# Kernel tuning notes

Hardware: AMD Instinct MI355X
Metric: run time of the kernel (lower is better)

## Reference

```python
import jax, jax.numpy as jnp
import numpy as np

# config (matches SS2Dv2 defaults: d_model=96, d_state=16, ssm_ratio=2.0, dt_rank=auto=6, k_group=4)
DM, DI, N, K, R = 96, 192, 16, 4, 6
BSZ, H_, W_ = 1, 56, 56


def setup_inputs() -> dict:
    key = jax.random.key(0)
    ks = jax.random.split(key, 8)
    return {
        "x": jax.random.normal(ks[0], (BSZ, H_, W_, DM), jnp.float32),
        "in_proj_w": jax.random.normal(ks[1], (2 * DI, DM), jnp.float32) / np.sqrt(DM).astype(np.float32),
        "conv_w": jax.random.normal(ks[2], (DI, 1, 3, 3), jnp.float32) * 0.1,
        "conv_b": jnp.zeros((DI,), jnp.float32),
        "x_proj_w": jax.random.normal(ks[3], (K, R + 2 * N, DI), jnp.float32) / np.sqrt(DI).astype(np.float32),
        "dt_projs_w": 0.1 * jax.random.uniform(ks[4], (K, DI, R), jnp.float32),
        "dt_projs_bias": 0.1 * jax.random.uniform(ks[5], (K, DI), jnp.float32),
        "A_logs": jnp.zeros((K * DI, N), jnp.float32),
        "Ds": jnp.ones((K * DI,), jnp.float32),
        "ln_w": jnp.ones((DI,), jnp.float32),
        "ln_b": jnp.zeros((DI,), jnp.float32),
        "out_proj_w": jax.random.normal(ks[6], (DM, DI), jnp.float32) / np.sqrt(DI).astype(np.float32),
    }


def _cross_scan(x):
    # x: (B, D, H, W) -> (B, 4, D, L); dirs: row-major, col-major, and their flips
    B, D, H, W = x.shape
    L = H * W
    x0 = x.reshape(B, D, L)
    x1 = jnp.swapaxes(x, 2, 3).reshape(B, D, L)
    return jnp.stack([x0, x1, x0[..., ::-1], x1[..., ::-1]], axis=1)


def _cross_merge(ys, H, W):
    # ys: (B, K, D, L) -> (B, D, L); invert each scan direction and sum
    B, Kk, D, L = ys.shape
    y0 = ys[:, 0]
    y2 = ys[:, 2][..., ::-1]
    y1 = jnp.swapaxes(ys[:, 1].reshape(B, D, W, H), 2, 3).reshape(B, D, L)
    y3 = jnp.swapaxes(ys[:, 3][..., ::-1].reshape(B, D, W, H), 2, 3).reshape(B, D, L)
    return y0 + y1 + y2 + y3


def _forward(x, in_proj_w, conv_w, conv_b, x_proj_w, dt_projs_w, dt_projs_bias,
             A_logs, Ds, ln_w, ln_b, out_proj_w):
    B, H, W, _ = x.shape
    L = H * W
    # in_proj + gate split (channel_first=False -> last dim)
    xz = jnp.einsum('bhwc,oc->bhwo', x, in_proj_w)
    xc, z = jnp.split(xz, 2, axis=-1)
    z = jax.nn.silu(z)
    # depthwise conv (NCHW)
    xc = jnp.transpose(xc, (0, 3, 1, 2))
    xc = jax.lax.conv_general_dilated(
        xc, conv_w, (1, 1), 'SAME', feature_group_count=DI,
        dimension_numbers=('NCHW', 'OIHW', 'NCHW')) + conv_b[None, :, None, None]
    xc = jax.nn.silu(xc)
    # 4-directional cross scan
    xs = _cross_scan(xc)  # (B,K,D,L)
    # grouped x_proj: per direction D -> R+2N
    x_dbl = jnp.einsum('bkdl,krd->bkrl', xs, x_proj_w)
    dts, Bs, Cs = jnp.split(x_dbl, [R, R + N], axis=2)  # (B,K,R,L),(B,K,N,L),(B,K,N,L)
    # grouped dt proj: per direction R -> D
    dts = jnp.einsum('bkrl,kdr->bkdl', dts, dt_projs_w)
    A = -jnp.exp(A_logs.astype(jnp.float32)).reshape(K, DI, N)
    delta = jax.nn.softplus(dts + dt_projs_bias[None, :, :, None])  # (B,K,D,L)
    # S6 selective scan: h_t = exp(delta*A)*h_{t-1} + delta*B*u, y_t = C.h_t + D*u
    dA = jnp.exp(jnp.einsum('bkdl,kdn->bkdln', delta, A))
    dBu = jnp.einsum('bkdl,bknl,bkdl->bkdln', delta, Bs, xs)

    def comb(e1, e2):
        a1, b1 = e1
        a2, b2 = e2
        return a2 * a1, a2 * b1 + b2

    _, h = jax.lax.associative_scan(comb, (dA, dBu), axis=3)  # (B,K,D,L,N)
    y = jnp.einsum('bkdln,bknl->bkdl', h, Cs) + Ds.reshape(K, DI)[None, :, :, None] * xs
    y = _cross_merge(y, H, W).reshape(B, DI, H, W)
    # out_norm: LayerNorm over channels (channel_first=False path)
    y = jnp.transpose(y, (0, 2, 3, 1))  # (B,H,W,D)
    mu = y.mean(-1, keepdims=True)
    var = ((y - mu) ** 2).mean(-1, keepdims=True)
    y = (y - mu) / jnp.sqrt(var + 1e-5) * ln_w + ln_b
    y = y * z
    return jnp.einsum('bhwd,od->bhwo', y, out_proj_w)


def reference(x, in_proj_w, conv_w, conv_b, x_proj_w, dt_projs_w, dt_projs_bias,
              A_logs, Ds, ln_w, ln_b, out_proj_w):
    return _forward(x, in_proj_w, conv_w, conv_b, x_proj_w, dt_projs_w, dt_projs_bias,
                    A_logs, Ds, ln_w, ln_b, out_proj_w)
```

## Files before the change

### kernel.cpp

```cpp
#include <hip/hip_runtime.h>
#include <hip/hip_bf16.h>
#include <math.h>

#define DM 96
#define DI 192
#define NS 16
#define KK 4
#define RR 6
#define HH 56
#define WW 56
#define LL (HH*WW)
#define RN (RR + 2*NS)
#define NCH 64
#define CLL (LL/NCH)

__device__ __forceinline__ float silu_f(float x) { return x / (1.f + __expf(-x)); }
__device__ __forceinline__ float softplus_f(float x) {
    return (x > 20.f) ? x : log1pf(__expf(x));
}

__global__ __launch_bounds__(256) void k_inproj(
        const float* __restrict__ x, const float* __restrict__ w,
        float* __restrict__ xc_t, float* __restrict__ z_nat) {
    __shared__ float xt[32 * 100];
    __shared__ float wt[32 * 100];
    const int l0 = blockIdx.x * 32;
    const int o0 = blockIdx.y * 32;
    const int tid = threadIdx.x;
    for (int i = tid; i < 32 * 24; i += 256) {
        int r = i / 24, q = i % 24;
        *(float4*)&xt[r * 100 + 4 * q] = *(const float4*)&x[(size_t)(l0 + r) * DM + 4 * q];
        *(float4*)&wt[r * 100 + 4 * q] = *(const float4*)&w[(size_t)(o0 + r) * DM + 4 * q];
    }
    __syncthreads();
    const int tx = tid & 15, ty = tid >> 4;
    float acc[2][2] = {};
    for (int c = 0; c < 96; c += 4) {
        float4 av[2], bv[2];
#pragma unroll
        for (int i = 0; i < 2; ++i) av[i] = *(const float4*)&xt[(ty + 16 * i) * 100 + c];
#pragma unroll
        for (int j = 0; j < 2; ++j) bv[j] = *(const float4*)&wt[(tx + 16 * j) * 100 + c];
#pragma unroll
        for (int i = 0; i < 2; ++i)
#pragma unroll
            for (int j = 0; j < 2; ++j) {
                acc[i][j] = fmaf(av[i].x, bv[j].x, acc[i][j]);
                acc[i][j] = fmaf(av[i].y, bv[j].y, acc[i][j]);
                acc[i][j] = fmaf(av[i].z, bv[j].z, acc[i][j]);
                acc[i][j] = fmaf(av[i].w, bv[j].w, acc[i][j]);
            }
    }
    __syncthreads();
    float* ot = xt;
#pragma unroll
    for (int j = 0; j < 2; ++j)
#pragma unroll
        for (int i = 0; i < 2; ++i)
            ot[(tx + 16 * j) * 65 + (ty + 16 * i)] = acc[i][j];
    __syncthreads();
    if (o0 < DI) {
        for (int i = tid; i < 32 * 32; i += 256) {
            int ol = i >> 5, ll = i & 31;
            xc_t[(size_t)(o0 + ol) * LL + l0 + ll] = ot[ol * 65 + ll];
        }
    } else {
        for (int i = tid; i < 32 * 32; i += 256) {
            int ll = i >> 5, ol = i & 31;
            z_nat[(size_t)(l0 + ll) * DI + (o0 - DI) + ol] = silu_f(ot[ol * 65 + ll]);
        }
    }
}

__global__ __launch_bounds__(256) void k_convT(
        const float* __restrict__ xc_t, const float* __restrict__ cw,
        const float* __restrict__ cb, float* __restrict__ xconv, float* __restrict__ xs1) {
    __shared__ float in_s[16 * 56];
    __shared__ float out_s[14 * 57];
    const int d = blockIdx.x;
    const int h0 = blockIdx.y * 14;
    const int tid = threadIdx.x;
    const float* in = xc_t + (size_t)d * LL;
    for (int i = tid; i < 16 * 14; i += 256) {
        int row = i / 14, q = i % 14;
        int r = row - 1 + h0;
        float4 v = make_float4(0.f, 0.f, 0.f, 0.f);
        if (r >= 0 && r < HH) v = *(const float4*)&in[r * WW + 4 * q];
        *(float4*)&in_s[row * 56 + 4 * q] = v;
    }
    __syncthreads();
    const float b0 = cb[d];
    float w9[9];
#pragma unroll
    for (int i = 0; i < 9; ++i) w9[i] = cw[d * 9 + i];
    for (int i = tid; i < 14 * 56; i += 256) {
        int hh = i / 56, w = i % 56;
        float acc = b0;
#pragma unroll
        for (int di = 0; di < 3; ++di)
#pragma unroll
            for (int dj = 0; dj < 3; ++dj) {
                int w2 = w + dj - 1;
                if (w2 < 0 || w2 >= WW) continue;
                acc = fmaf(in_s[(hh + di) * 56 + w2], w9[di * 3 + dj], acc);
            }
        acc = silu_f(acc);
        xconv[(size_t)d * LL + (h0 + hh) * WW + w] = acc;
        out_s[hh * 57 + w] = acc;
    }
    __syncthreads();
    for (int i = tid; i < 14 * 56; i += 256) {
        int w = i / 14, hh = i % 14;
        xs1[(size_t)d * LL + w * HH + h0 + hh] = out_s[hh * 57 + w];
    }
}

__global__ __launch_bounds__(256) void k_xdblD(
        const float* __restrict__ xconv, const float* __restrict__ xs1,
        const float* __restrict__ pw, const float* __restrict__ dtw,
        const float* __restrict__ dtb,
        float* __restrict__ Bn, float* __restrict__ Cn, float* __restrict__ delta) {
    __shared__ float xt[DI * 16];
    __shared__ float wk_s[32 * DI];
    __shared__ float dtS[RR * 17];
    const int k = blockIdx.y;
    const int l0 = blockIdx.x * 16;
    const int tid = threadIdx.x;
    const float* in = (k & 1) ? xs1 : xconv;
    const float* wk = pw + (size_t)k * RN * DI;
    for (int i = tid; i < DI * 4; i += 256) {
        int d = i >> 2, q = i & 3;
        *(float4*)&xt[(d << 4) + 4 * q] = *(const float4*)&in[(size_t)d * LL + l0 + 4 * q];
    }
    {
        const float4* src = (const float4*)(wk + RR * DI);
        float4* dst = (float4*)wk_s;
        for (int i = tid; i < (32 * DI) / 4; i += 256) dst[i] = src[i];
    }
    __syncthreads();
    if (tid < RR * 16) {
        int r = tid >> 4, lx = tid & 15;
        const float* wr = wk + r * DI;
        float acc = 0.f;
#pragma unroll 8
        for (int d = 0; d < DI; ++d) acc = fmaf(xt[(d << 4) + lx], wr[d], acc);
        dtS[r * 17 + lx] = acc;
    }
    {
        const int sx = tid & 15, cg = tid >> 4;
        float acc2[2] = {};
        for (int d = 0; d < DI; d += 4) {
            float x0 = xt[(d + 0) * 16 + sx];
            float x1 = xt[(d + 1) * 16 + sx];
            float x2 = xt[(d + 2) * 16 + sx];
            float x3 = xt[(d + 3) * 16 + sx];
#pragma unroll
            for (int j = 0; j < 2; ++j) {
                float4 wv = *(const float4*)&wk_s[(cg + 16 * j) * DI + d];
                acc2[j] = fmaf(x0, wv.x, acc2[j]);
                acc2[j] = fmaf(x1, wv.y, acc2[j]);
                acc2[j] = fmaf(x2, wv.z, acc2[j]);
                acc2[j] = fmaf(x3, wv.w, acc2[j]);
            }
        }
        int s = l0 + sx;
        int ss = (k < 2) ? s : (LL - 1 - s);
        int cch = ss / CLL, ttl = ss - cch * CLL;
        size_t idx = ((size_t)k * LL + (size_t)ttl * NCH + cch) * NS + cg;
        Bn[idx] = acc2[0];
        Cn[idx] = acc2[1];
    }
    __syncthreads();
    for (int oi = tid; oi < DI * 16; oi += 256) {
        int d = oi >> 4, sl = oi & 15;
        int kd = k * DI + d;
        const float* wr = dtw + (size_t)kd * RR;
        float acc = dtb[kd];
#pragma unroll
        for (int r = 0; r < RR; ++r) acc = fmaf(dtS[r * 17 + sl], wr[r], acc);
        delta[(size_t)kd * LL + l0 + sl] = softplus_f(acc);
    }
}

template<int STP, bool TRANS>
__device__ __forceinline__ void scan_dir(
        const float* sDel, const float* sU,
        const float* __restrict__ pB, const float* __restrict__ pC,
        float4 An, float Dv, int c, int n,
        float* __restrict__ sP, float* __restrict__ sH,
        float* __restrict__ yo0,
        float* ysm,
        int im0) {
    float sd = 0.f;
    float4 h = make_float4(0.f, 0.f, 0.f, 0.f);
#pragma unroll 7
    for (int tl = 0; tl < CLL; ++tl) {
        float dl = sDel[STP * tl];
        float u  = sU[STP * tl];
        float4 Bv = *(const float4*)&pB[(size_t)tl * (NCH * NS)];
        float du = dl * u;
        h.x = fmaf(__builtin_amdgcn_exp2f(dl * An.x), h.x, du * Bv.x);
        h.y = fmaf(__builtin_amdgcn_exp2f(dl * An.y), h.y, du * Bv.y);
        h.z = fmaf(__builtin_amdgcn_exp2f(dl * An.z), h.z, du * Bv.z);
        h.w = fmaf(__builtin_amdgcn_exp2f(dl * An.w), h.w, du * Bv.w);
        sd += dl;
    }
    *(float4*)&sP[c * NS + 4 * n] = make_float4(
        __builtin_amdgcn_exp2f(sd * An.x), __builtin_amdgcn_exp2f(sd * An.y),
        __builtin_amdgcn_exp2f(sd * An.z), __builtin_amdgcn_exp2f(sd * An.w));
    *(float4*)&sH[c * NS + 4 * n] = h;
    __syncthreads();
    float4 hin = make_float4(0.f, 0.f, 0.f, 0.f);
    for (int cc = 0; cc < c; ++cc) {
        float4 P  = *(const float4*)&sP[cc * NS + 4 * n];
        float4 Hh = *(const float4*)&sH[cc * NS + 4 * n];
        hin.x = fmaf(P.x, hin.x, Hh.x);
        hin.y = fmaf(P.y, hin.y, Hh.y);
        hin.z = fmaf(P.z, hin.z, Hh.z);
        hin.w = fmaf(P.w, hin.w, Hh.w);
    }

    float4 h2 = hin;
    float yreg[13];
#pragma unroll 7
    for (int tl = 0; tl < CLL; ++tl) {
        float dl = sDel[STP * tl];
        float u  = sU[STP * tl];
        float4 Bv = *(const float4*)&pB[(size_t)tl * (NCH * NS)];
        float4 Cv = *(const float4*)&pC[(size_t)tl * (NCH * NS)];
        float du = dl * u;
        h2.x = fmaf(__builtin_amdgcn_exp2f(dl * An.x), h2.x, du * Bv.x);
        h2.y = fmaf(__builtin_amdgcn_exp2f(dl * An.y), h2.y, du * Bv.y);
        h2.z = fmaf(__builtin_amdgcn_exp2f(dl * An.z), h2.z, du * Bv.z);
        h2.w = fmaf(__builtin_amdgcn_exp2f(dl * An.w), h2.w, du * Bv.w);
        float acc = h2.x * Cv.x;
        acc = fmaf(h2.y, Cv.y, acc);
        acc = fmaf(h2.z, Cv.z, acc);
        acc = fmaf(h2.w, Cv.w, acc);
        acc += __shfl_xor(acc, 2, 64);
        acc += __shfl_xor(acc, 1, 64);
        acc = fmaf(Dv, u, acc);
        if ((tl & 3) == n) yreg[tl >> 2] = acc;
    }
    if (!TRANS) {
#pragma unroll
        for (int j = 0; j < 12; ++j)
            yo0[STP * (j * 4 + n)] = yreg[j];
        if (n == 0)
            yo0[STP * 48] = yreg[12];
    } else {
        __syncthreads();
#pragma unroll
        for (int j = 0; j < 12; ++j) {
            int im = im0 + STP * (j * 4 + n);
            int w = im / HH, hh = im - w * HH;
            ysm[hh * 57 + w] = yreg[j];
        }
        if (n == 0) {
            int im = im0 + STP * 48;
            int w = im / HH, hh = im - w * HH;
            ysm[hh * 57 + w] = yreg[12];
        }
    }
}

__global__ __launch_bounds__(256) void k_scan(
        const float* __restrict__ delta, const float* __restrict__ Bn,
        const float* __restrict__ Cn,
        const float* __restrict__ xconv, const float* __restrict__ xs1,
        const float* __restrict__ A_logs, const float* __restrict__ Ds,
        float* __restrict__ y4) {
    __shared__ float sbuf[2 * LL];
    __shared__ float sP[NCH * NS];
    __shared__ float sH[NCH * NS];
    int b = blockIdx.x;
    int k = b / DI, d = b % DI;
    int tid = threadIdx.x;
    int c = tid >> 2, n = tid & 3;
    int kd = k * DI + d;
    const float LOG2E = 1.4426950408889634f;
    float4 Alg = *(const float4*)&A_logs[kd * NS + 4 * n];
    float4 An = make_float4(-__expf(Alg.x) * LOG2E, -__expf(Alg.y) * LOG2E,
                            -__expf(Alg.z) * LOG2E, -__expf(Alg.w) * LOG2E);
    float Dv = Ds[kd];
    const float* del = delta + (size_t)kd * LL;
    const float* uP  = ((k & 1) ? xs1 : xconv) + (size_t)d * LL;
    {
        const float4* s1 = (const float4*)del;
        const float4* s2 = (const float4*)uP;
        float4* d1 = (float4*)sbuf;
        float4* d2 = (float4*)(sbuf + LL);
        for (int i = tid; i < LL / 4; i += 256) {
            d1[i] = s1[i];
            d2[i] = s2[i];
        }
    }
    __syncthreads();
    const float* Bb = Bn + (size_t)k * LL * NS + c * NS + 4 * n;
    const float* Cb = Cn + (size_t)k * LL * NS + c * NS + 4 * n;
    float* yo = y4 + (size_t)kd * LL;
    const int t0 = c * CLL;
    const int imF = t0;
    const int imR = LL - 1 - t0;
    if (k == 0) {
        scan_dir<1, false>(sbuf + imF, sbuf + LL + imF, Bb, Cb,
                           An, Dv, c, n, sP, sH, yo + imF, nullptr, 0);
    } else if (k == 1) {
        scan_dir<1, true>(sbuf + imF, sbuf + LL + imF, Bb, Cb,
                          An, Dv, c, n, sP, sH, nullptr, sbuf, imF);
    } else if (k == 2) {
        scan_dir<-1, false>(sbuf + imR, sbuf + LL + imR, Bb, Cb,
                            An, Dv, c, n, sP, sH, yo + imR, nullptr, 0);
    } else {
        scan_dir<-1, true>(sbuf + imR, sbuf + LL + imR, Bb, Cb,
                           An, Dv, c, n, sP, sH, nullptr, sbuf, imR);
    }
    if (k & 1) {
        __syncthreads();
        for (int p = tid; p < LL; p += 256)
            yo[p] = sbuf[p + p / WW];
    }
}

__global__ __launch_bounds__(256) void k_lnout(
        const float* __restrict__ y4, const float* __restrict__ z_nat,
        const float* __restrict__ lnw, const float* __restrict__ lnb,
        const float* __restrict__ ow, float* __restrict__ out) {
    __shared__ float yv[16 * 196];
    __shared__ float ow_s[48 * 196];
    __shared__ float mean_s[16], inv_s[16];
    const int l0 = blockIdx.x * 16;
    const int tid = threadIdx.x;
    for (int i = tid; i < DI * 4; i += 256) {
        int d = i >> 2, q = i & 3;
        size_t off = (size_t)d * LL + l0 + 4 * q;
        float4 a = *(const float4*)&y4[off];
        float4 b = *(const float4*)&y4[(size_t)DI * LL + off];
        float4 c2 = *(const float4*)&y4[(size_t)(2 * DI) * LL + off];
        float4 e = *(const float4*)&y4[(size_t)(3 * DI) * LL + off];
        int p = 4 * q;
        yv[(p + 0) * 196 + d] = a.x + b.x + c2.x + e.x;
        yv[(p + 1) * 196 + d] = a.y + b.y + c2.y + e.y;
        yv[(p + 2) * 196 + d] = a.z + b.z + c2.z + e.z;
        yv[(p + 3) * 196 + d] = a.w + b.w + c2.w + e.w;
    }
    __syncthreads();
    {
        int p = tid >> 4, e = tid & 15;
        float s1 = 0.f;
#pragma unroll
        for (int m = 0; m < 12; ++m) s1 += yv[p * 196 + e + 16 * m];
        s1 += __shfl_xor(s1, 8, 64);
        s1 += __shfl_xor(s1, 4, 64);
        s1 += __shfl_xor(s1, 2, 64);
        s1 += __shfl_xor(s1, 1, 64);
        float mean = s1 * (1.f / DI);
        float s2 = 0.f;
#pragma unroll
        for (int m = 0; m < 12; ++m) {
            float dv = yv[p * 196 + e + 16 * m] - mean;
            s2 = fmaf(dv, dv, s2);
        }
        s2 += __shfl_xor(s2, 8, 64);
        s2 += __shfl_xor(s2, 4, 64);
        s2 += __shfl_xor(s2, 2, 64);
        s2 += __shfl_xor(s2, 1, 64);
        if (e == 0) {
            mean_s[p] = mean;
            inv_s[p] = rsqrtf(s2 * (1.f / DI) + 1e-5f);
        }
    }
    __syncthreads();
    for (int i = tid; i < 16 * 48; i += 256) {
        int p = i / 48, q = i % 48;
        float4 z4 = *(const float4*)&z_nat[(size_t)(l0 + p) * DI + 4 * q];
        float4 w4 = *(const float4*)&lnw[4 * q];
        float4 b4 = *(const float4*)&lnb[4 * q];
        float4 yy = *(const float4*)&yv[p * 196 + 4 * q];
        float m = mean_s[p], iv = inv_s[p];
        yy.x = ((yy.x - m) * iv * w4.x + b4.x) * z4.x;
        yy.y = ((yy.y - m) * iv * w4.y + b4.y) * z4.y;
        yy.z = ((yy.z - m) * iv * w4.z + b4.z) * z4.z;
        yy.w = ((yy.w - m) * iv * w4.w + b4.w) * z4.w;
        *(float4*)&yv[p * 196 + 4 * q] = yy;
    }
    const int ty = tid >> 4, tx = tid & 15;
#pragma unroll
    for (int pass = 0; pass < 2; ++pass) {
        __syncthreads();
        for (int i = tid; i < 48 * 48; i += 256) {
            int o = i / 48, q = i % 48;
            *(float4*)&ow_s[o * 196 + 4 * q] =
                *(const float4*)&ow[(size_t)(pass * 48 + o) * DI + 4 * q];
        }
        __syncthreads();
        float acc[3] = {};
        for (int dd = 0; dd < DI; dd += 4) {
            float4 a0 = *(const float4*)&yv[ty * 196 + dd];
#pragma unroll
            for (int j = 0; j < 3; ++j) {
                float4 bv = *(const float4*)&ow_s[(tx + 16 * j) * 196 + dd];
                acc[j] += a0.x * bv.x + a0.y * bv.y + a0.z * bv.z + a0.w * bv.w;
            }
        }
#pragma unroll
        for (int j = 0; j < 3; ++j)
            out[(size_t)(l0 + ty) * DM + pass * 48 + tx + 16 * j] = acc[j];
    }
}

extern "C" void kernel_launch(void* const* d_in, const int* in_sizes, int n_in,
                              void* d_out, int out_size, void* d_ws, size_t ws_size,
                              hipStream_t stream) {
    const float* x    = (const float*)d_in[0];
    const float* ipw  = (const float*)d_in[1];
    const float* cw   = (const float*)d_in[2];
    const float* cb   = (const float*)d_in[3];
    const float* xpw  = (const float*)d_in[4];
    const float* dtw  = (const float*)d_in[5];
    const float* dtb  = (const float*)d_in[6];
    const float* alog = (const float*)d_in[7];
    const float* Dsp  = (const float*)d_in[8];
    const float* lnw  = (const float*)d_in[9];
    const float* lnb  = (const float*)d_in[10];
    const float* ow   = (const float*)d_in[11];
    float* out = (float*)d_out;

    float* ws     = (float*)d_ws;
    float* xc_t   = ws;
    float* z_nat  = xc_t + DI * LL;
    float* xconv  = z_nat + DI * LL;
    float* xs1    = xconv + DI * LL;
    float* Bn     = xs1 + DI * LL;
    float* Cn     = Bn + (size_t)KK * LL * NS;
    float* delta  = Cn + (size_t)KK * LL * NS;
    float* y4     = delta + (size_t)KK * DI * LL;

    k_inproj <<<dim3(LL / 32, 12), 256, 0, stream>>>(x, ipw, xc_t, z_nat);
    k_convT  <<<dim3(DI, 4), 256, 0, stream>>>(xc_t, cw, cb, xconv, xs1);
    k_xdblD  <<<dim3(LL / 16, KK), 256, 0, stream>>>(xconv, xs1, xpw, dtw, dtb, Bn, Cn, delta);
    k_scan   <<<KK * DI, 256, 0, stream>>>(delta, Bn, Cn, xconv, xs1, alog, Dsp, y4);
    k_lnout  <<<LL / 16, 256, 0, stream>>>(y4, z_nat, lnw, lnb, ow, out);
}
```

Baseline: 163.1 us.

## Process two channels per scan block and split out-proj passes across grid

Each scan block now handles two adjacent channels of the same direction, sharing the B/C loads from global memory and doubling the independent recurrence chains per thread to hide exp/FMA latency. Shared memory for the scan grows to four sequences (about 50 KB plus carry buffers), which can lower occupancy, and the block count is halved to 384. Separately, the LayerNorm+out-proj kernel gets a second grid dimension so each block computes one 48-column half of the output. That doubles the y4 reduction and LayerNorm work but removes the serial second pass and lets the weight load overlap the y4 load.

```diff
diff --git a/kernel.cpp b/kernel.cpp
--- a/kernel.cpp
+++ b/kernel.cpp
@@ -183,83 +183,121 @@
 }
 
 template<int STP, bool TRANS>
-__device__ __forceinline__ void scan_dir(
-        const float* sDel, const float* sU,
+__device__ __forceinline__ void scan_dir2(
+        const float* sD0, const float* sU0,
+        const float* sD1, const float* sU1,
         const float* __restrict__ pB, const float* __restrict__ pC,
-        float4 An, float Dv, int c, int n,
+        float4 An0, float4 An1, float Dv0, float Dv1, int c, int n,
         float* __restrict__ sP, float* __restrict__ sH,
-        float* __restrict__ yo0,
-        float* ysm,
+        float* __restrict__ yg0, float* __restrict__ yg1,
+        float* ys0, float* ys1,
         int im0) {
-    float sd = 0.f;
-    float4 h = make_float4(0.f, 0.f, 0.f, 0.f);
+    float sd0 = 0.f, sd1 = 0.f;
+    float4 h0 = make_float4(0.f, 0.f, 0.f, 0.f);
+    float4 h1 = make_float4(0.f, 0.f, 0.f, 0.f);
 #pragma unroll 7
     for (int tl = 0; tl < CLL; ++tl) {
-        float dl = sDel[STP * tl];
-        float u  = sU[STP * tl];
+        float dl0 = sD0[STP * tl], u0 = sU0[STP * tl];
+        float dl1 = sD1[STP * tl], u1 = sU1[STP * tl];
         float4 Bv = *(const float4*)&pB[(size_t)tl * (NCH * NS)];
-        float du = dl * u;
-        h.x = fmaf(__builtin_amdgcn_exp2f(dl * An.x), h.x, du * Bv.x);
-        h.y = fmaf(__builtin_amdgcn_exp2f(dl * An.y), h.y, du * Bv.y);
-        h.z = fmaf(__builtin_amdgcn_exp2f(dl * An.z), h.z, du * Bv.z);
-        h.w = fmaf(__builtin_amdgcn_exp2f(dl * An.w), h.w, du * Bv.w);
-        sd += dl;
+        float du0 = dl0 * u0, du1 = dl1 * u1;
+        h0.x = fmaf(__builtin_amdgcn_exp2f(dl0 * An0.x), h0.x, du0 * Bv.x);
+        h0.y = fmaf(__builtin_amdgcn_exp2f(dl0 * An0.y), h0.y, du0 * Bv.y);
+        h0.z = fmaf(__builtin_amdgcn_exp2f(dl0 * An0.z), h0.z, du0 * Bv.z);
+        h0.w = fmaf(__builtin_amdgcn_exp2f(dl0 * An0.w), h0.w, du0 * Bv.w);
+        h1.x = fmaf(__builtin_amdgcn_exp2f(dl1 * An1.x), h1.x, du1 * Bv.x);
+        h1.y = fmaf(__builtin_amdgcn_exp2f(dl1 * An1.y), h1.y, du1 * Bv.y);
+        h1.z = fmaf(__builtin_amdgcn_exp2f(dl1 * An1.z), h1.z, du1 * Bv.z);
+        h1.w = fmaf(__builtin_amdgcn_exp2f(dl1 * An1.w), h1.w, du1 * Bv.w);
+        sd0 += dl0; sd1 += dl1;
     }
     *(float4*)&sP[c * NS + 4 * n] = make_float4(
-        __builtin_amdgcn_exp2f(sd * An.x), __builtin_amdgcn_exp2f(sd * An.y),
-        __builtin_amdgcn_exp2f(sd * An.z), __builtin_amdgcn_exp2f(sd * An.w));
-    *(float4*)&sH[c * NS + 4 * n] = h;
-    __syncthreads();
-    float4 hin = make_float4(0.f, 0.f, 0.f, 0.f);
+        __builtin_amdgcn_exp2f(sd0 * An0.x), __builtin_amdgcn_exp2f(sd0 * An0.y),
+        __builtin_amdgcn_exp2f(sd0 * An0.z), __builtin_amdgcn_exp2f(sd0 * An0.w));
+    *(float4*)&sH[c * NS + 4 * n] = h0;
+    __syncthreads();
+    float4 hin0 = make_float4(0.f, 0.f, 0.f, 0.f);
     for (int cc = 0; cc < c; ++cc) {
         float4 P  = *(const float4*)&sP[cc * NS + 4 * n];
         float4 Hh = *(const float4*)&sH[cc * NS + 4 * n];
-        hin.x = fmaf(P.x, hin.x, Hh.x);
-        hin.y = fmaf(P.y, hin.y, Hh.y);
-        hin.z = fmaf(P.z, hin.z, Hh.z);
-        hin.w = fmaf(P.w, hin.w, Hh.w);
-    }
-
-    float4 h2 = hin;
-    float yreg[13];
+        hin0.x = fmaf(P.x, hin0.x, Hh.x);
+        hin0.y = fmaf(P.y, hin0.y, Hh.y);
+        hin0.z = fmaf(P.z, hin0.z, Hh.z);
+        hin0.w = fmaf(P.w, hin0.w, Hh.w);
+    }
+    __syncthreads();
+    *(float4*)&sP[c * NS + 4 * n] = make_float4(
+        __builtin_amdgcn_exp2f(sd1 * An1.x), __builtin_amdgcn_exp2f(sd1 * An1.y),
+        __builtin_amdgcn_exp2f(sd1 * An1.z), __builtin_amdgcn_exp2f(sd1 * An1.w));
+    *(float4*)&sH[c * NS + 4 * n] = h1;
+    __syncthreads();
+    float4 hin1 = make_float4(0.f, 0.f, 0.f, 0.f);
+    for (int cc = 0; cc < c; ++cc) {
+        float4 P  = *(const float4*)&sP[cc * NS + 4 * n];
+        float4 Hh = *(const float4*)&sH[cc * NS + 4 * n];
+        hin1.x = fmaf(P.x, hin1.x, Hh.x);
+        hin1.y = fmaf(P.y, hin1.y, Hh.y);
+        hin1.z = fmaf(P.z, hin1.z, Hh.z);
+        hin1.w = fmaf(P.w, hin1.w, Hh.w);
+    }
+
+    float4 h20 = hin0, h21 = hin1;
+    float yr0[13], yr1[13];
 #pragma unroll 7
     for (int tl = 0; tl < CLL; ++tl) {
-        float dl = sDel[STP * tl];
-        float u  = sU[STP * tl];
+        float dl0 = sD0[STP * tl], u0 = sU0[STP * tl];
+        float dl1 = sD1[STP * tl], u1 = sU1[STP * tl];
         float4 Bv = *(const float4*)&pB[(size_t)tl * (NCH * NS)];
         float4 Cv = *(const float4*)&pC[(size_t)tl * (NCH * NS)];
-        float du = dl * u;
-        h2.x = fmaf(__builtin_amdgcn_exp2f(dl * An.x), h2.x, du * Bv.x);
-        h2.y = fmaf(__builtin_amdgcn_exp2f(dl * An.y), h2.y, du * Bv.y);
-        h2.z = fmaf(__builtin_amdgcn_exp2f(dl * An.z), h2.z, du * Bv.z);
-        h2.w = fmaf(__builtin_amdgcn_exp2f(dl * An.w), h2.w, du * Bv.w);
-        float acc = h2.x * Cv.x;
-        acc = fmaf(h2.y, Cv.y, acc);
-        acc = fmaf(h2.z, Cv.z, acc);
-        acc = fmaf(h2.w, Cv.w, acc);
-        acc += __shfl_xor(acc, 2, 64);
-        acc += __shfl_xor(acc, 1, 64);
-        acc = fmaf(Dv, u, acc);
-        if ((tl & 3) == n) yreg[tl >> 2] = acc;
+        float du0 = dl0 * u0, du1 = dl1 * u1;
+        h20.x = fmaf(__builtin_amdgcn_exp2f(dl0 * An0.x), h20.x, du0 * Bv.x);
+        h20.y = fmaf(__builtin_amdgcn_exp2f(dl0 * An0.y), h20.y, du0 * Bv.y);
+        h20.z = fmaf(__builtin_amdgcn_exp2f(dl0 * An0.z), h20.z, du0 * Bv.z);
+        h20.w = fmaf(__builtin_amdgcn_exp2f(dl0 * An0.w), h20.w, du0 * Bv.w);
+        h21.x = fmaf(__builtin_amdgcn_exp2f(dl1 * An1.x), h21.x, du1 * Bv.x);
+        h21.y = fmaf(__builtin_amdgcn_exp2f(dl1 * An1.y), h21.y, du1 * Bv.y);
+        h21.z = fmaf(__builtin_amdgcn_exp2f(dl1 * An1.z), h21.z, du1 * Bv.z);
+        h21.w = fmaf(__builtin_amdgcn_exp2f(dl1 * An1.w), h21.w, du1 * Bv.w);
+        float a0 = h20.x * Cv.x;
+        a0 = fmaf(h20.y, Cv.y, a0);
+        a0 = fmaf(h20.z, Cv.z, a0);
+        a0 = fmaf(h20.w, Cv.w, a0);
+        float a1 = h21.x * Cv.x;
+        a1 = fmaf(h21.y, Cv.y, a1);
+        a1 = fmaf(h21.z, Cv.z, a1);
+        a1 = fmaf(h21.w, Cv.w, a1);
+        a0 += __shfl_xor(a0, 2, 64);
+        a0 += __shfl_xor(a0, 1, 64);
+        a1 += __shfl_xor(a1, 2, 64);
+        a1 += __shfl_xor(a1, 1, 64);
+        a0 = fmaf(Dv0, u0, a0);
+        a1 = fmaf(Dv1, u1, a1);
+        if ((tl & 3) == n) { yr0[tl >> 2] = a0; yr1[tl >> 2] = a1; }
     }
     if (!TRANS) {
 #pragma unroll
-        for (int j = 0; j < 12; ++j)
-            yo0[STP * (j * 4 + n)] = yreg[j];
-        if (n == 0)
-            yo0[STP * 48] = yreg[12];
+        for (int j = 0; j < 12; ++j) {
+            yg0[STP * (j * 4 + n)] = yr0[j];
+            yg1[STP * (j * 4 + n)] = yr1[j];
+        }
+        if (n == 0) {
+            yg0[STP * 48] = yr0[12];
+            yg1[STP * 48] = yr1[12];
+        }
     } else {
         __syncthreads();
 #pragma unroll
         for (int j = 0; j < 12; ++j) {
             int im = im0 + STP * (j * 4 + n);
             int w = im / HH, hh = im - w * HH;
-            ysm[hh * 57 + w] = yreg[j];
+            ys0[hh * 57 + w] = yr0[j];
+            ys1[hh * 57 + w] = yr1[j];
         }
         if (n == 0) {
             int im = im0 + STP * 48;
             int w = im / HH, hh = im - w * HH;
-            ysm[hh * 57 + w] = yreg[12];
+            ys0[hh * 57 + w] = yr0[12];
+            ys1[hh * 57 + w] = yr1[12];
         }
     }
 }
@@ -270,55 +308,71 @@
         const float* __restrict__ xconv, const float* __restrict__ xs1,
         const float* __restrict__ A_logs, const float* __restrict__ Ds,
         float* __restrict__ y4) {
-    __shared__ float sbuf[2 * LL];
+    __shared__ float sbuf[4 * LL];
     __shared__ float sP[NCH * NS];
     __shared__ float sH[NCH * NS];
     int b = blockIdx.x;
-    int k = b / DI, d = b % DI;
+    int k = b / (DI / 2), dp = b % (DI / 2);
+    int d0 = 2 * dp;
     int tid = threadIdx.x;
     int c = tid >> 2, n = tid & 3;
-    int kd = k * DI + d;
+    int kd0 = k * DI + d0;
     const float LOG2E = 1.4426950408889634f;
-    float4 Alg = *(const float4*)&A_logs[kd * NS + 4 * n];
-    float4 An = make_float4(-__expf(Alg.x) * LOG2E, -__expf(Alg.y) * LOG2E,
-                            -__expf(Alg.z) * LOG2E, -__expf(Alg.w) * LOG2E);
-    float Dv = Ds[kd];
-    const float* del = delta + (size_t)kd * LL;
-    const float* uP  = ((k & 1) ? xs1 : xconv) + (size_t)d * LL;
+    float4 Alg0 = *(const float4*)&A_logs[(size_t)kd0 * NS + 4 * n];
+    float4 Alg1 = *(const float4*)&A_logs[(size_t)(kd0 + 1) * NS + 4 * n];
+    float4 An0 = make_float4(-__expf(Alg0.x) * LOG2E, -__expf(Alg0.y) * LOG2E,
+                             -__expf(Alg0.z) * LOG2E, -__expf(Alg0.w) * LOG2E);
+    float4 An1 = make_float4(-__expf(Alg1.x) * LOG2E, -__expf(Alg1.y) * LOG2E,
+                             -__expf(Alg1.z) * LOG2E, -__expf(Alg1.w) * LOG2E);
+    float Dv0 = Ds[kd0], Dv1 = Ds[kd0 + 1];
+    const float* del0 = delta + (size_t)kd0 * LL;
+    const float* uP0  = ((k & 1) ? xs1 : xconv) + (size_t)d0 * LL;
     {
-        const float4* s1 = (const float4*)del;
-        const float4* s2 = (const float4*)uP;
-        float4* d1 = (float4*)sbuf;
-        float4* d2 = (float4*)(sbuf + LL);
-        for (int i = tid; i < LL / 4; i += 256) {
-            d1[i] = s1[i];
-            d2[i] = s2[i];
+        const float4* s1 = (const float4*)del0;
+        const float4* s2 = (const float4*)uP0;
+        float4* dst = (float4*)sbuf;
+        for (int i = tid; i < LL / 2; i += 256) {
+            dst[i] = s1[i];
+            dst[LL / 2 + i] = s2[i];
         }
     }
     __syncthreads();
     const float* Bb = Bn + (size_t)k * LL * NS + c * NS + 4 * n;
     const float* Cb = Cn + (size_t)k * LL * NS + c * NS + 4 * n;
-    float* yo = y4 + (size_t)kd * LL;
+    float* yo0 = y4 + (size_t)kd0 * LL;
+    float* yo1 = yo0 + LL;
+    float* ys0 = sbuf;
+    float* ys1 = sbuf + 57 * 56;
     const int t0 = c * CLL;
     const int imF = t0;
     const int imR = LL - 1 - t0;
+    const float* sD0 = sbuf;
+    const float* sD1 = sbuf + LL;
+    const float* sU0 = sbuf + 2 * LL;
+    const float* sU1 = sbuf + 3 * LL;
     if (k == 0) {
-        scan_dir<1, false>(sbuf + imF, sbuf + LL + imF, Bb, Cb,
-                           An, Dv, c, n, sP, sH, yo + imF, nullptr, 0);
+        scan_dir2<1, false>(sD0 + imF, sU0 + imF, sD1 + imF, sU1 + imF, Bb, Cb,
+                            An0, An1, Dv0, Dv1, c, n, sP, sH,
+                            yo0 + imF, yo1 + imF, nullptr, nullptr, 0);
     } else if (k == 1) {
-        scan_dir<1, true>(sbuf + imF, sbuf + LL + imF, Bb, Cb,
-                          An, Dv, c, n, sP, sH, nullptr, sbuf, imF);
+        scan_dir2<1, true>(sD0 + imF, sU0 + imF, sD1 + imF, sU1 + imF, Bb, Cb,
+                           An0, An1, Dv0, Dv1, c, n, sP, sH,
+                           nullptr, nullptr, ys0, ys1, imF);
     } else if (k == 2) {
-        scan_dir<-1, false>(sbuf + imR, sbuf + LL + imR, Bb, Cb,
-                            An, Dv, c, n, sP, sH, yo + imR, nullptr, 0);
+        scan_dir2<-1, false>(sD0 + imR, sU0 + imR, sD1 + imR, sU1 + imR, Bb, Cb,
+                             An0, An1, Dv0, Dv1, c, n, sP, sH,
+                             yo0 + imR, yo1 + imR, nullptr, nullptr, 0);
     } else {
-        scan_dir<-1, true>(sbuf + imR, sbuf + LL + imR, Bb, Cb,
-                           An, Dv, c, n, sP, sH, nullptr, sbuf, imR);
+        scan_dir2<-1, true>(sD0 + imR, sU0 + imR, sD1 + imR, sU1 + imR, Bb, Cb,
+                            An0, An1, Dv0, Dv1, c, n, sP, sH,
+                            nullptr, nullptr, ys0, ys1, imR);
     }
     if (k & 1) {
         __syncthreads();
-        for (int p = tid; p < LL; p += 256)
-            yo[p] = sbuf[p + p / WW];
+        for (int p = tid; p < LL; p += 256) {
+            yo0[p] = ys0[p + p / WW];
+            yo1[p] = ys1[p + p / WW];
+        }
     }
 }
 
@@ -330,7 +384,13 @@
     __shared__ float ow_s[48 * 196];
     __shared__ float mean_s[16], inv_s[16];
     const int l0 = blockIdx.x * 16;
+    const int pass = blockIdx.y;
     const int tid = threadIdx.x;
+    for (int i = tid; i < 48 * 48; i += 256) {
+        int o = i / 48, q = i % 48;
+        *(float4*)&ow_s[o * 196 + 4 * q] =
+            *(const float4*)&ow[(size_t)(pass * 48 + o) * DI + 4 * q];
+    }
     for (int i = tid; i < DI * 4; i += 256) {
         int d = i >> 2, q = i & 3;
         size_t off = (size_t)d * LL + l0 + 4 * q;
@@ -384,29 +444,20 @@
         yy.w = ((yy.w - m) * iv * w4.w + b4.w) * z4.w;
         *(float4*)&yv[p * 196 + 4 * q] = yy;
     }
+    __syncthreads();
     const int ty = tid >> 4, tx = tid & 15;
-#pragma unroll
-    for (int pass = 0; pass < 2; ++pass) {
-        __syncthreads();
-        for (int i = tid; i < 48 * 48; i += 256) {
-            int o = i / 48, q = i % 48;
-            *(float4*)&ow_s[o * 196 + 4 * q] =
-                *(const float4*)&ow[(size_t)(pass * 48 + o) * DI + 4 * q];
-        }
-        __syncthreads();
-        float acc[3] = {};
-        for (int dd = 0; dd < DI; dd += 4) {
-            float4 a0 = *(const float4*)&yv[ty * 196 + dd];
-#pragma unroll
-            for (int j = 0; j < 3; ++j) {
-                float4 bv = *(const float4*)&ow_s[(tx + 16 * j) * 196 + dd];
-                acc[j] += a0.x * bv.x + a0.y * bv.y + a0.z * bv.z + a0.w * bv.w;
-            }
-        }
-#pragma unroll
-        for (int j = 0; j < 3; ++j)
-            out[(size_t)(l0 + ty) * DM + pass * 48 + tx + 16 * j] = acc[j];
-    }
+    float acc[3] = {};
+    for (int dd = 0; dd < DI; dd += 4) {
+        float4 a0 = *(const float4*)&yv[ty * 196 + dd];
+#pragma unroll
+        for (int j = 0; j < 3; ++j) {
+            float4 bv = *(const float4*)&ow_s[(tx + 16 * j) * 196 + dd];
+            acc[j] += a0.x * bv.x + a0.y * bv.y + a0.z * bv.z + a0.w * bv.w;
+        }
+    }
+#pragma unroll
+    for (int j = 0; j < 3; ++j)
+        out[(size_t)(l0 + ty) * DM + pass * 48 + tx + 16 * j] = acc[j];
 }
 
 extern "C" void kernel_launch(void* const* d_in, const int* in_sizes, int n_in,
@@ -439,6 +490,6 @@
     k_inproj <<<dim3(LL / 32, 12), 256, 0, stream>>>(x, ipw, xc_t, z_nat);
     k_convT  <<<dim3(DI, 4), 256, 0, stream>>>(xc_t, cw, cb, xconv, xs1);
     k_xdblD  <<<dim3(LL / 16, KK), 256, 0, stream>>>(xconv, xs1, xpw, dtw, dtb, Bn, Cn, delta);
-    k_scan   <<<KK * DI, 256, 0, stream>>>(delta, Bn, Cn, xconv, xs1, alog, Dsp, y4);
-    k_lnout  <<<LL / 16, 256, 0, stream>>>(y4, z_nat, lnw, lnb, ow, out);
-}
+    k_scan   <<<KK * DI / 2, 256, 0, stream>>>(delta, Bn, Cn, xconv, xs1, alog, Dsp, y4);
+    k_lnout  <<<dim3(LL / 16, 2), 256, 0, stream>>>(y4, z_nat, lnw, lnb, ow, out);
+}
```

Measured after the change: 173.8 us. +6.5%, slower.

## Double-buffer B/C register prefetch in chunked scan loops and raise occupancy hint

Applied to the files above, without the earlier changes.

Both chunk scan passes now load the B (and C) float4 vectors for the next group of 7 timesteps into a register buffer while computing on the current group, giving software-pipelined global-load latency hiding. The launch bounds for k_scan add a minimum of 3 blocks per CU. The change spends many more VGPRs on prefetch buffers, and the occupancy hint may force spills or limit unrolling. Since yreg indexing now uses fully unrolled constant indices, it may stay in registers.

```diff
diff --git a/kernel.cpp b/kernel.cpp
--- a/kernel.cpp
+++ b/kernel.cpp
@@ -193,17 +193,33 @@
         int im0) {
     float sd = 0.f;
     float4 h = make_float4(0.f, 0.f, 0.f, 0.f);
-#pragma unroll 7
-    for (int tl = 0; tl < CLL; ++tl) {
-        float dl = sDel[STP * tl];
-        float u  = sU[STP * tl];
-        float4 Bv = *(const float4*)&pB[(size_t)tl * (NCH * NS)];
-        float du = dl * u;
-        h.x = fmaf(__builtin_amdgcn_exp2f(dl * An.x), h.x, du * Bv.x);
-        h.y = fmaf(__builtin_amdgcn_exp2f(dl * An.y), h.y, du * Bv.y);
-        h.z = fmaf(__builtin_amdgcn_exp2f(dl * An.z), h.z, du * Bv.z);
-        h.w = fmaf(__builtin_amdgcn_exp2f(dl * An.w), h.w, du * Bv.w);
-        sd += dl;
+    {
+        float4 qb[2][7];
+#pragma unroll
+        for (int j = 0; j < 7; ++j)
+            qb[0][j] = *(const float4*)&pB[(size_t)j * (NCH * NS)];
+#pragma unroll
+        for (int w = 0; w < 7; ++w) {
+            if (w < 6) {
+#pragma unroll
+                for (int j = 0; j < 7; ++j)
+                    qb[(w + 1) & 1][j] =
+                        *(const float4*)&pB[(size_t)((w + 1) * 7 + j) * (NCH * NS)];
+            }
+#pragma unroll
+            for (int j = 0; j < 7; ++j) {
+                const int tl = w * 7 + j;
+                float dl = sDel[STP * tl];
+                float u  = sU[STP * tl];
+                float du = dl * u;
+                const float4 Bv = qb[w & 1][j];
+                h.x = fmaf(__builtin_amdgcn_exp2f(dl * An.x), h.x, du * Bv.x);
+                h.y = fmaf(__builtin_amdgcn_exp2f(dl * An.y), h.y, du * Bv.y);
+                h.z = fmaf(__builtin_amdgcn_exp2f(dl * An.z), h.z, du * Bv.z);
+                h.w = fmaf(__builtin_amdgcn_exp2f(dl * An.w), h.w, du * Bv.w);
+                sd += dl;
+            }
+        }
     }
     *(float4*)&sP[c * NS + 4 * n] = make_float4(
         __builtin_amdgcn_exp2f(sd * An.x), __builtin_amdgcn_exp2f(sd * An.y),
@@ -222,25 +238,46 @@
 
     float4 h2 = hin;
     float yreg[13];
-#pragma unroll 7
-    for (int tl = 0; tl < CLL; ++tl) {
-        float dl = sDel[STP * tl];
-        float u  = sU[STP * tl];
-        float4 Bv = *(const float4*)&pB[(size_t)tl * (NCH * NS)];
-        float4 Cv = *(const float4*)&pC[(size_t)tl * (NCH * NS)];
-        float du = dl * u;
-        h2.x = fmaf(__builtin_amdgcn_exp2f(dl * An.x), h2.x, du * Bv.x);
-        h2.y = fmaf(__builtin_amdgcn_exp2f(dl * An.y), h2.y, du * Bv.y);
-        h2.z = fmaf(__builtin_amdgcn_exp2f(dl * An.z), h2.z, du * Bv.z);
-        h2.w = fmaf(__builtin_amdgcn_exp2f(dl * An.w), h2.w, du * Bv.w);
-        float acc = h2.x * Cv.x;
-        acc = fmaf(h2.y, Cv.y, acc);
-        acc = fmaf(h2.z, Cv.z, acc);
-        acc = fmaf(h2.w, Cv.w, acc);
-        acc += __shfl_xor(acc, 2, 64);
-        acc += __shfl_xor(acc, 1, 64);
-        acc = fmaf(Dv, u, acc);
-        if ((tl & 3) == n) yreg[tl >> 2] = acc;
+    {
+        float4 pb[2][7], pc[2][7];
+#pragma unroll
+        for (int j = 0; j < 7; ++j) {
+            pb[0][j] = *(const float4*)&pB[(size_t)j * (NCH * NS)];
+            pc[0][j] = *(const float4*)&pC[(size_t)j * (NCH * NS)];
+        }
+#pragma unroll
+        for (int w = 0; w < 7; ++w) {
+            if (w < 6) {
+#pragma unroll
+                for (int j = 0; j < 7; ++j) {
+                    pb[(w + 1) & 1][j] =
+                        *(const float4*)&pB[(size_t)((w + 1) * 7 + j) * (NCH * NS)];
+                    pc[(w + 1) & 1][j] =
+                        *(const float4*)&pC[(size_t)((w + 1) * 7 + j) * (NCH * NS)];
+                }
+            }
+#pragma unroll
+            for (int j = 0; j < 7; ++j) {
+                const int tl = w * 7 + j;
+                float dl = sDel[STP * tl];
+                float u  = sU[STP * tl];
+                float du = dl * u;
+                const float4 Bv = pb[w & 1][j];
+                const float4 Cv = pc[w & 1][j];
+                h2.x = fmaf(__builtin_amdgcn_exp2f(dl * An.x), h2.x, du * Bv.x);
+                h2.y = fmaf(__builtin_amdgcn_exp2f(dl * An.y), h2.y, du * Bv.y);
+                h2.z = fmaf(__builtin_amdgcn_exp2f(dl * An.z), h2.z, du * Bv.z);
+                h2.w = fmaf(__builtin_amdgcn_exp2f(dl * An.w), h2.w, du * Bv.w);
+                float acc = h2.x * Cv.x;
+                acc = fmaf(h2.y, Cv.y, acc);
+                acc = fmaf(h2.z, Cv.z, acc);
+                acc = fmaf(h2.w, Cv.w, acc);
+                acc += __shfl_xor(acc, 2, 64);
+                acc += __shfl_xor(acc, 1, 64);
+                acc = fmaf(Dv, u, acc);
+                if ((tl & 3) == n) yreg[tl >> 2] = acc;
+            }
+        }
     }
     if (!TRANS) {
 #pragma unroll
@@ -264,7 +301,7 @@
     }
 }
 
-__global__ __launch_bounds__(256) void k_scan(
+__global__ __launch_bounds__(256, 3) void k_scan(
         const float* __restrict__ delta, const float* __restrict__ Bn,
         const float* __restrict__ Cn,
         const float* __restrict__ xconv, const float* __restrict__ xs1,
```

New measurement: 158.8 us. 2.7% less time.
